# Optimization experiments

Hardware: AMD Instinct MI355X
Metric: run time of the kernel (lower is better)

Reference implementation:

```python
import jax, jax.numpy as jnp
import numpy as np

D_MODEL = 512
N_HEADS = 8
D_FF = 1024
LV = 2048
LT = 512
GAMMA = 0.9
SCALE_BASE = 512  # XPOS default scale_base


def _dup_interleave(m):
    # (L, d/2) -> (L, d) duplicating each column: [a,b] -> [a,a,b,b]
    return jnp.repeat(m, 2, axis=-1)


def _xpos(x, downscale=False):
    # XPOS rotary embedding (RetNet-style), x: (B, L, d)
    B, L, d = x.shape
    half = d // 2
    s = (jnp.arange(0, d, 2, dtype=jnp.float32) + 0.4 * d) / (1.4 * d)  # (d/2,)
    scale = s[None, :] ** (jnp.arange(L, dtype=jnp.float32)[:, None] / SCALE_BASE)  # (L, d/2)
    inv_freq = 1.0 / (10000.0 ** (jnp.arange(half, dtype=jnp.float32) / half))
    ang = jnp.arange(L, dtype=jnp.float32)[:, None] * inv_freq[None, :]  # (L, d/2)
    if downscale:
        scale = 1.0 / scale
    sin = _dup_interleave(jnp.sin(ang) * scale)[None]  # (1, L, d)
    cos = _dup_interleave(jnp.cos(ang) * scale)[None]
    x1, x2 = x[..., 0::2], x[..., 1::2]
    rot = jnp.stack((-x2, x1), axis=-1).reshape(x.shape)  # rotate_every_two
    return x * cos + rot * sin


def _sine_pos(L, d):
    # DETR-style normalized 1D sine position embedding, mask = ones(1, L)
    x_embed = jnp.arange(1, L + 1, dtype=jnp.float32)  # cumsum of ones
    x_embed = x_embed / (x_embed[-1] + 1e-6) * (2.0 * np.pi)
    dim_t = jnp.arange(d, dtype=jnp.float32)
    dim_t = 10000.0 ** (2.0 * jnp.floor(dim_t / 2.0) / d)
    pos = x_embed[:, None] / dim_t[None, :]  # (L, d)
    pos = jnp.stack((jnp.sin(pos[:, 0::2]), jnp.cos(pos[:, 1::2])), axis=2).reshape(L, d)
    return pos[None]  # (1, L, d)


def _ln(x, w, b, eps=1e-5):
    mu = jnp.mean(x, axis=-1, keepdims=True)
    var = jnp.var(x, axis=-1, keepdims=True)
    return (x - mu) / jnp.sqrt(var + eps) * w + b


def _ret_forward(src_vid, src_txt, ln1_w, ln1_b, wq, bq, wk, bk, wv, bv, wo, bo,
                 lin1_w, lin1_b, lin2_w, lin2_b, ln2_w, ln2_b, ln3_w, ln3_b,
                 learn_ret_w):
    B, Lv, D = src_vid.shape
    Lt = src_txt.shape[1]
    h, dk = N_HEADS, D // N_HEADS

    # retention decay matrix D[n,m] = gamma^(n-m) for n>=m else 0
    n = jnp.arange(Lv)
    delta = jnp.maximum(n[:, None] - n[None, :], 0).astype(jnp.float32)
    Dm = jnp.where(n[:, None] >= n[None, :], GAMMA ** delta, 0.0)

    # learned sparse mask
    learn = jax.nn.sigmoid(learn_ret_w.reshape(Lv, Lv))
    diag = jnp.eye(Lv, dtype=jnp.float32)
    video_ret = (1.0 - diag) * learn
    learn_mask = diag + video_ret
    mask = Dm * learn_mask  # mask_choice == 'both'
    loss_sparsity = jnp.mean(jnp.abs(video_ret))

    # position encodings
    pos_vid_q = _xpos(src_vid)
    pos_vid_k = _xpos(src_vid, downscale=True)
    pos_txt = _sine_pos(Lt, D)
    src = jnp.concatenate([src_vid, src_txt], axis=1)       # (B, Lv+Lt, D)
    pos = jnp.concatenate([pos_vid_q, pos_txt], axis=1)
    pos_k = jnp.concatenate([pos_vid_k, pos_txt], axis=1)

    # --- RetLayer (eval mode: dropout = identity) ---
    src2 = _ln(src, ln1_w, ln1_b)
    q = src2[:, :Lv] + pos[:, :Lv]
    k = src2[:, :Lv] + pos_k[:, :Lv]
    v = src2[:, :Lv]

    # multi-head attention with MULTIPLICATIVE mask on logits
    qh = (q @ wq.T + bq).reshape(B, Lv, h, dk) / jnp.sqrt(jnp.float32(dk))
    kh = (k @ wk.T + bk).reshape(B, Lv, h, dk)
    vh = (v @ wv.T + bv).reshape(B, Lv, h, dk)
    attn = jnp.einsum('blhd,bmhd->bhlm', qh, kh) * mask[None, None]
    attn = jax.nn.softmax(attn, axis=-1)
    vid_att = jnp.einsum('bhlm,bmhd->blhd', attn, vh).reshape(B, Lv, D)
    vid_att = vid_att @ wo.T + bo

    src2 = jnp.concatenate([vid_att, src2[:, Lv:]], axis=1) + pos
    src = src + src2
    src2 = _ln(src, ln2_w, ln2_b)
    src2 = jax.nn.gelu(src2 @ lin1_w.T + lin1_b, approximate=False) @ lin2_w.T + lin2_b
    src = src + src2
    src = _ln(src, ln3_w, ln3_b)
    return src[:, :Lv], src[:, Lv:], loss_sparsity


def setup_inputs() -> dict:
    key = jax.random.key(0)
    ks = jax.random.split(key, 12)
    D, F = D_MODEL, D_FF
    w = lambda k, shp: (jax.random.normal(k, shp, dtype=jnp.float32) * 0.02)
    return {
        'src_vid': jax.random.normal(ks[0], (1, LV, D), dtype=jnp.float32),
        'src_txt': jax.random.normal(ks[1], (1, LT, D), dtype=jnp.float32),
        'ln1_w': jnp.ones((D,), jnp.float32), 'ln1_b': jnp.zeros((D,), jnp.float32),
        'wq': w(ks[2], (D, D)), 'bq': jnp.zeros((D,), jnp.float32),
        'wk': w(ks[3], (D, D)), 'bk': jnp.zeros((D,), jnp.float32),
        'wv': w(ks[4], (D, D)), 'bv': jnp.zeros((D,), jnp.float32),
        'wo': w(ks[5], (D, D)), 'bo': jnp.zeros((D,), jnp.float32),
        'lin1_w': w(ks[6], (F, D)), 'lin1_b': jnp.zeros((F,), jnp.float32),
        'lin2_w': w(ks[7], (D, F)), 'lin2_b': jnp.zeros((D,), jnp.float32),
        'ln2_w': jnp.ones((D,), jnp.float32), 'ln2_b': jnp.zeros((D,), jnp.float32),
        'ln3_w': jnp.ones((D,), jnp.float32), 'ln3_b': jnp.zeros((D,), jnp.float32),
        'learn_ret_w': jax.random.normal(ks[8], (LV * LV,), dtype=jnp.float32),
    }


def reference(src_vid, src_txt, ln1_w, ln1_b, wq, bq, wk, bk, wv, bv, wo, bo,
              lin1_w, lin1_b, lin2_w, lin2_b, ln2_w, ln2_b, ln3_w, ln3_b,
              learn_ret_w):
    return _ret_forward(src_vid, src_txt, ln1_w, ln1_b, wq, bq, wk, bk, wv, bv,
                        wo, bo, lin1_w, lin1_b, lin2_w, lin2_b, ln2_w, ln2_b,
                        ln3_w, ln3_b, learn_ret_w)
```

## Files before the change

### kernel.cpp

```cpp
#include <hip/hip_runtime.h>
#include <hip/hip_bf16.h>
#include <math.h>

#define LVID 2048
#define LTXT 512
#define DMOD 512
#define LTOT 2560
#define LOG2_GAMMA (-0.15200309344504995f)
#define LOG2E 1.4426950408889634f

typedef __bf16 bf16x8 __attribute__((ext_vector_type(8)));
typedef float f32x4 __attribute__((ext_vector_type(4)));

__device__ inline f32x4 mfma_bf16(bf16x8 a, bf16x8 b, f32x4 c) {
  return __builtin_amdgcn_mfma_f32_16x16x32_bf16(a, b, c, 0, 0, 0);
}

__device__ inline void gload_lds16(const void* g, void* l) {
  __builtin_amdgcn_global_load_lds(
      (const __attribute__((address_space(1))) void*)g,
      (__attribute__((address_space(3))) void*)l, 16, 0, 0);
}

union U8 { __hip_bfloat16 b[8]; uint4 u; };

__global__ __launch_bounds__(256) void k_prep_ln1(
    const float* __restrict__ lw, float* __restrict__ premask2,
    float* __restrict__ lossp,
    const float* __restrict__ wq, const float* __restrict__ wk,
    const float* __restrict__ wv, const float* __restrict__ wo,
    const float* __restrict__ l1, const float* __restrict__ l2,
    __hip_bfloat16* __restrict__ dst,
    const float* __restrict__ src_vid, const float* __restrict__ src_txt,
    const float* __restrict__ w, const float* __restrict__ b,
    __hip_bfloat16* __restrict__ acat, float* __restrict__ srcA,
    float* __restrict__ posb) {
  int tid = threadIdx.x;
  int blk = blockIdx.x;
  if (blk < 2048) {
    __shared__ float red[256];
    int idx0 = (blk * 256 + tid) * 8;
    int i = idx0 >> 11, j0 = idx0 & 2047;
    float4 lv0 = *(const float4*)&lw[idx0];
    float4 lv1 = *(const float4*)&lw[idx0 + 4];
    float lvv[8] = {lv0.x, lv0.y, lv0.z, lv0.w, lv1.x, lv1.y, lv1.z, lv1.w};
    float pm[8];
    float s = 0.f;
#pragma unroll
    for (int e = 0; e < 8; e++) {
      int j = j0 + e;
      float sig = 1.f / (1.f + __expf(-lvv[e]));
      if (j != i) s += sig;
      float m = (j > i) ? 0.f
              : ((j == i) ? 1.f : exp2f((float)(i - j) * LOG2_GAMMA) * sig);
      pm[e] = m * LOG2E;
    }
    *(float4*)&premask2[idx0]     = *(float4*)&pm[0];
    *(float4*)&premask2[idx0 + 4] = *(float4*)&pm[4];
    red[tid] = s; __syncthreads();
    for (int st = 128; st > 0; st >>= 1) { if (tid < st) red[tid] += red[tid + st]; __syncthreads(); }
    if (tid == 0) lossp[blk] = red[0];
  } else if (blk < 4096) {
    int i4 = (blk - 2048) * 256 + tid;
    const float* sp; int base;
    if (i4 < 131072)      { if (i4 < 65536)  { sp = wq; base = 0; }      else { sp = wk; base = 65536; } }
    else if (i4 < 262144) { if (i4 < 196608) { sp = wv; base = 131072; } else { sp = wo; base = 196608; } }
    else if (i4 < 393216) { sp = l1; base = 262144; }
    else                  { sp = l2; base = 393216; }
    float4 v = ((const float4*)sp)[i4 - base];
    __hip_bfloat16 o[4] = {__float2bfloat16(v.x), __float2bfloat16(v.y),
                           __float2bfloat16(v.z), __float2bfloat16(v.w)};
    *(uint2*)(dst + (size_t)i4 * 4) = *(uint2*)o;
  } else {
    int row = (blk - 4096) * 4 + (tid >> 6);
    int lane = tid & 63;
    const float* xs = (row < LVID) ? (src_vid + (size_t)row * DMOD)
                                   : (src_txt + (size_t)(row - LVID) * DMOD);
    float x[8];
    { float4 v0 = *(const float4*)&xs[lane * 8];
      float4 v1 = *(const float4*)&xs[lane * 8 + 4];
      x[0]=v0.x; x[1]=v0.y; x[2]=v0.z; x[3]=v0.w;
      x[4]=v1.x; x[5]=v1.y; x[6]=v1.z; x[7]=v1.w; }
    float s = 0.f;
#pragma unroll
    for (int i = 0; i < 8; i++) s += x[i];
#pragma unroll
    for (int st = 1; st < 64; st <<= 1) s += __shfl_xor(s, st, 64);
    float mu = s * (1.f / DMOD);
    float vs = 0.f;
#pragma unroll
    for (int i = 0; i < 8; i++) { float d = x[i] - mu; vs += d * d; }
#pragma unroll
    for (int st = 1; st < 64; st <<= 1) vs += __shfl_xor(vs, st, 64);
    float inv = rsqrtf(vs * (1.f / DMOD) + 1e-5f);
    float y[8];
    { float4 w0 = *(const float4*)&w[lane * 8];
      float4 w1 = *(const float4*)&w[lane * 8 + 4];
      float4 b0 = *(const float4*)&b[lane * 8];
      float4 b1 = *(const float4*)&b[lane * 8 + 4];
      float wv_[8] = {w0.x,w0.y,w0.z,w0.w,w1.x,w1.y,w1.z,w1.w};
      float bv_[8] = {b0.x,b0.y,b0.z,b0.w,b1.x,b1.y,b1.z,b1.w};
#pragma unroll
      for (int i = 0; i < 8; i++) y[i] = (x[i] - mu) * inv * wv_[i] + bv_[i]; }
    size_t base = (size_t)row * DMOD + lane * 8;
    if (row < LVID) {
      U8 pv;
#pragma unroll
      for (int i = 0; i < 8; i++) pv.b[i] = __float2bfloat16(y[i]);
      *(uint4*)&acat[(size_t)(4096 + row) * DMOD + lane * 8] = pv.u;
      float pq[8], pk[8];
      float l = (float)row;
#pragma unroll
      for (int p = 0; p < 4; p++) {
        int j = lane * 4 + p;
        float sj = (2.f * j + 204.8f) * (1.f / 716.8f);
        float scale = __powf(sj, l * (1.f / 512.f));
        float invfreq = __powf(10000.f, -(float)j * (1.f / 256.f));
        float sn, cs; __sincosf(l * invfreq, &sn, &cs);
        float cq = cs * scale, sq = sn * scale;
        pq[2*p]   = x[2*p] * cq - x[2*p+1] * sq;
        pq[2*p+1] = x[2*p+1] * cq + x[2*p] * sq;
        float isc = 1.f / scale;
        float ck = cs * isc, sk = sn * isc;
        pk[2*p]   = x[2*p] * ck - x[2*p+1] * sk;
        pk[2*p+1] = x[2*p+1] * ck + x[2*p] * sk;
      }
      *(float4*)&posb[base]     = *(float4*)&pq[0];
      *(float4*)&posb[base + 4] = *(float4*)&pq[4];
      U8 pqv, pkv;
#pragma unroll
      for (int i = 0; i < 8; i++) {
        pqv.b[i] = __float2bfloat16(y[i] + pq[i]);
        pkv.b[i] = __float2bfloat16(y[i] + pk[i]);
      }
      *(uint4*)&acat[(size_t)row * DMOD + lane * 8] = pqv.u;
      *(uint4*)&acat[(size_t)(2048 + row) * DMOD + lane * 8] = pkv.u;
    } else {
      int l = row - LVID;
      float xe = (float)(l + 1) * (6.28318530717958647692f / 512.000001f);
      float o8[8];
#pragma unroll
      for (int p = 0; p < 4; p++) {
        int j = lane * 4 + p;
        float dimt = __powf(10000.f, (float)j * (1.f / 256.f));
        float a = xe / dimt;
        o8[2*p]   = x[2*p]   + y[2*p]   + __sinf(a);
        o8[2*p+1] = x[2*p+1] + y[2*p+1] + __cosf(a);
      }
      *(float4*)&srcA[base]     = *(float4*)&o8[0];
      *(float4*)&srcA[base + 4] = *(float4*)&o8[4];
    }
  }
}

__global__ __launch_bounds__(256) void k_ln2(
    const float* __restrict__ srcA,
    const float* __restrict__ w, const float* __restrict__ b,
    __hip_bfloat16* __restrict__ obf) {
  int row = blockIdx.x * 4 + (threadIdx.x >> 6);
  int lane = threadIdx.x & 63;
  size_t base = (size_t)row * DMOD + lane * 8;
  float x[8];
  { float4 v0 = *(const float4*)&srcA[base];
    float4 v1 = *(const float4*)&srcA[base + 4];
    x[0]=v0.x; x[1]=v0.y; x[2]=v0.z; x[3]=v0.w;
    x[4]=v1.x; x[5]=v1.y; x[6]=v1.z; x[7]=v1.w; }
  float s = 0.f;
#pragma unroll
  for (int i = 0; i < 8; i++) s += x[i];
#pragma unroll
  for (int st = 1; st < 64; st <<= 1) s += __shfl_xor(s, st, 64);
  float mu = s * (1.f / DMOD);
  float vs = 0.f;
#pragma unroll
  for (int i = 0; i < 8; i++) { float d = x[i] - mu; vs += d * d; }
#pragma unroll
  for (int st = 1; st < 64; st <<= 1) vs += __shfl_xor(vs, st, 64);
  float inv = rsqrtf(vs * (1.f / DMOD) + 1e-5f);
  float4 w0 = *(const float4*)&w[lane * 8];
  float4 w1 = *(const float4*)&w[lane * 8 + 4];
  float4 b0 = *(const float4*)&b[lane * 8];
  float4 b1 = *(const float4*)&b[lane * 8 + 4];
  float wv_[8] = {w0.x,w0.y,w0.z,w0.w,w1.x,w1.y,w1.z,w1.w};
  float bv_[8] = {b0.x,b0.y,b0.z,b0.w,b1.x,b1.y,b1.z,b1.w};
  U8 o;
#pragma unroll
  for (int i = 0; i < 8; i++)
    o.b[i] = __float2bfloat16((x[i] - mu) * inv * wv_[i] + bv_[i]);
  *(uint4*)&obf[base] = o.u;
}

__global__ __launch_bounds__(256) void k_ln3(
    const float* __restrict__ srcA, const float* __restrict__ ffo0,
    const float* __restrict__ ffo1,
    const float* __restrict__ w, const float* __restrict__ b,
    float* __restrict__ o, const float* __restrict__ lossp) {
  if (blockIdx.x == 0 && threadIdx.x < 64) {
    float s = 0.f;
    for (int i = threadIdx.x; i < 2048; i += 64) s += lossp[i];
#pragma unroll
    for (int st = 1; st < 64; st <<= 1) s += __shfl_xor(s, st, 64);
    if (threadIdx.x == 0) o[1310720] = s * (1.f / 4194304.f);
  }
  int row = blockIdx.x * 4 + (threadIdx.x >> 6);
  int lane = threadIdx.x & 63;
  size_t base = (size_t)row * DMOD + lane * 8;
  float x[8];
  { float4 a0 = *(const float4*)&srcA[base];
    float4 a1 = *(const float4*)&srcA[base + 4];
    float4 f0 = *(const float4*)&ffo0[base];
    float4 f1 = *(const float4*)&ffo0[base + 4];
    float4 g0 = *(const float4*)&ffo1[base];
    float4 g1 = *(const float4*)&ffo1[base + 4];
    x[0]=a0.x+f0.x+g0.x; x[1]=a0.y+f0.y+g0.y; x[2]=a0.z+f0.z+g0.z; x[3]=a0.w+f0.w+g0.w;
    x[4]=a1.x+f1.x+g1.x; x[5]=a1.y+f1.y+g1.y; x[6]=a1.z+f1.z+g1.z; x[7]=a1.w+f1.w+g1.w; }
  float s = 0.f;
#pragma unroll
  for (int i = 0; i < 8; i++) s += x[i];
#pragma unroll
  for (int st = 1; st < 64; st <<= 1) s += __shfl_xor(s, st, 64);
  float mu = s * (1.f / DMOD);
  float vs = 0.f;
#pragma unroll
  for (int i = 0; i < 8; i++) { float d = x[i] - mu; vs += d * d; }
#pragma unroll
  for (int st = 1; st < 64; st <<= 1) vs += __shfl_xor(vs, st, 64);
  float inv = rsqrtf(vs * (1.f / DMOD) + 1e-5f);
  float4 w0 = *(const float4*)&w[lane * 8];
  float4 w1 = *(const float4*)&w[lane * 8 + 4];
  float4 b0 = *(const float4*)&b[lane * 8];
  float4 b1 = *(const float4*)&b[lane * 8 + 4];
  float wv_[8] = {w0.x,w0.y,w0.z,w0.w,w1.x,w1.y,w1.z,w1.w};
  float bv_[8] = {b0.x,b0.y,b0.z,b0.w,b1.x,b1.y,b1.z,b1.w};
  float y[8];
#pragma unroll
  for (int i = 0; i < 8; i++) y[i] = (x[i] - mu) * inv * wv_[i] + bv_[i];
  *(float4*)&o[base]     = *(float4*)&y[0];
  *(float4*)&o[base + 4] = *(float4*)&y[4];
}

template <int EPI>
__global__ __launch_bounds__(256) void k_gemm4(
    const __hip_bfloat16* __restrict__ A, const __hip_bfloat16* __restrict__ W0,
    const float* __restrict__ b0, const float* __restrict__ b1,
    const float* __restrict__ b2, void* __restrict__ Cv,
    const float* __restrict__ res1, const float* __restrict__ res2,
    float* __restrict__ vtot, int M, int N, int K) {
  __shared__ __hip_bfloat16 sA[2][2048];
  __shared__ __hip_bfloat16 sB[2][2048];
  int tid = threadIdx.x, lane = tid & 63, w = tid >> 6;
  int c16 = lane & 15, q4 = lane >> 4;
  int bm = blockIdx.y * 64, bn = blockIdx.x * 64;
  int seg = (EPI == 3) ? (bm >> 11) : 0;
  const __hip_bfloat16* Wp = (EPI == 3) ? (W0 + (size_t)seg * ((size_t)N * K)) : W0;
  int kb   = (EPI == 5) ? (int)blockIdx.z * (K >> 1) : 0;
  int Keff = (EPI == 5) ? (K >> 1) : K;
  int r0 = tid >> 2, cc0 = (tid & 3) * 8;
  const __hip_bfloat16* gA = A  + (size_t)(bm + r0) * K + kb + cc0;
  const __hip_bfloat16* gB = Wp + (size_t)(bn + r0) * K + kb + cc0;
  auto stage = [&](int buf, int k0) {
    gload_lds16(gA + k0, &sA[buf][(size_t)tid * 8]);
    gload_lds16(gB + k0, &sB[buf][(size_t)tid * 8]);
  };
  f32x4 acc[2][2];
  { f32x4 z = {0.f,0.f,0.f,0.f}; acc[0][0]=z; acc[0][1]=z; acc[1][0]=z; acc[1][1]=z; }
  int wm = w & 1, wn = w >> 1;
  const int S = Keff >> 5;
  stage(0, 0);
  for (int s = 0; s < S; s++) {
    __syncthreads();
    if (s + 1 < S) stage((s + 1) & 1, (s + 1) * 32);
    int bf = s & 1;
    bf16x8 af[2], bfr[2];
    af[0]  = *(const bf16x8*)&sA[bf][(wm*32 + c16) * 32 + q4*8];
    af[1]  = *(const bf16x8*)&sA[bf][(wm*32 + 16 + c16) * 32 + q4*8];
    bfr[0] = *(const bf16x8*)&sB[bf][(wn*32 + c16) * 32 + q4*8];
    bfr[1] = *(const bf16x8*)&sB[bf][(wn*32 + 16 + c16) * 32 + q4*8];
    acc[0][0] = mfma_bf16(af[0], bfr[0], acc[0][0]);
    acc[0][1] = mfma_bf16(af[0], bfr[1], acc[0][1]);
    acc[1][0] = mfma_bf16(af[1], bfr[0], acc[1][0]);
    acc[1][1] = mfma_bf16(af[1], bfr[1], acc[1][1]);
  }
  float alpha = (EPI == 3 && seg == 0) ? 0.125f : 1.f;
  const float* bp = (EPI == 3) ? (seg == 0 ? b0 : (seg == 1 ? b1 : b2)) : b0;
  float vsum[2] = {0.f, 0.f};
#pragma unroll
  for (int j = 0; j < 2; j++) {
    int n = bn + wn*32 + j*16 + c16;
    float bs = bp[n];
    if (EPI == 5 && blockIdx.z != 0) bs = 0.f;
#pragma unroll
    for (int i = 0; i < 2; i++) {
#pragma unroll
      for (int r = 0; r < 4; r++) {
        int m = bm + wm*32 + i*16 + q4*4 + r;
        float v = (acc[i][j][r] + bs) * alpha;
        if (EPI == 4) v = 0.5f * v * (1.f + erff(v * 0.70710678118654752f));
        if (EPI == 2) {
          size_t off = (size_t)m * N + n;
          ((float*)Cv)[off] = v + res1[off] + res2[off];
        } else if (EPI == 4) {
          ((__hip_bfloat16*)Cv)[(size_t)m * N + n] = __float2bfloat16(v);
        } else if (EPI == 5) {
          ((float*)Cv)[(size_t)blockIdx.z * 1310720 + (size_t)m * N + n] = v;
        } else {
          __hip_bfloat16 vb = __float2bfloat16(v);
          ((__hip_bfloat16*)Cv)[(size_t)(m & 2047) * 1536 + seg * 512 + n] = vb;
          if (seg == 2) vsum[j] += __bfloat162float(vb);
        }
      }
    }
  }
  if (EPI == 3 && seg == 2) {
#pragma unroll
    for (int j = 0; j < 2; j++) {
      float s2 = vsum[j];
      s2 += __shfl_xor(s2, 16, 64);
      s2 += __shfl_xor(s2, 32, 64);
      if (q4 == 0) atomicAdd(&vtot[bn + wn*32 + j*16 + c16], s2);
    }
  }
}

__global__ __launch_bounds__(256) void k_attn(
    const __hip_bfloat16* __restrict__ qkv,
    const float* __restrict__ premask2,
    const float* __restrict__ Vtot,
    __hip_bfloat16* __restrict__ outp) {
  __shared__ __hip_bfloat16 sQ[64][72];
  __shared__ __hip_bfloat16 sK[2][64][72];
  __shared__ __hip_bfloat16 sVt[2][64][72];
  __shared__ __hip_bfloat16 sP[64][72];
  __shared__ float sVa[4][64];
  int i0 = blockIdx.x * 64, h = blockIdx.y;
  int tid = threadIdx.x, lane = tid & 63, w = tid >> 6;
  int c16 = lane & 15, q4 = lane >> 4;
  {
    int r = tid >> 2, c0 = (tid & 3) * 16;
    const __hip_bfloat16* g = qkv + (size_t)(i0 + r) * 1536 + h * 64 + c0;
    *(uint4*)&sQ[r][c0]     = *(const uint4*)g;
    *(uint4*)&sQ[r][c0 + 8] = *(const uint4*)(g + 8);
  }
  int thi = i0 >> 6;
  int tlo = (i0 > 900) ? ((i0 - 900) >> 6) : 0;
  float rm = 0.f, rz = 0.f;
  f32x4 O[4];
  { f32x4 z = {0.f,0.f,0.f,0.f}; O[0]=z; O[1]=z; O[2]=z; O[3]=z; }
  float vacc = 0.f;
  int kr = tid >> 2, kc = (tid & 3) * 16;
  uint4 pk0, pk1;
  U8 pv0, pv1;
  {
    const __hip_bfloat16* gk = qkv + (size_t)(tlo*64 + kr) * 1536 + 512 + h*64 + kc;
    pk0 = *(const uint4*)gk; pk1 = *(const uint4*)(gk + 8);
    const __hip_bfloat16* gv = qkv + (size_t)(tlo*64 + w*16) * 1536 + 1024 + h*64 + lane;
#pragma unroll
    for (int j = 0; j < 8; j++) pv0.b[j] = gv[(size_t)j * 1536];
#pragma unroll
    for (int j = 0; j < 8; j++) pv1.b[j] = gv[(size_t)(j + 8) * 1536];
  }
  for (int t = tlo; t <= thi; t++) {
    int buf = (t - tlo) & 1;
    *(uint4*)&sK[buf][kr][kc]       = pk0;
    *(uint4*)&sK[buf][kr][kc + 8]   = pk1;
    *(uint4*)&sVt[buf][lane][w*16]     = pv0.u;
    *(uint4*)&sVt[buf][lane][w*16 + 8] = pv1.u;
#pragma unroll
    for (int j = 0; j < 8; j++) vacc += __bfloat162float(pv0.b[j]);
#pragma unroll
    for (int j = 0; j < 8; j++) vacc += __bfloat162float(pv1.b[j]);
    __syncthreads();
    if (t < thi) {
      const __hip_bfloat16* gk = qkv + (size_t)((t+1)*64 + kr) * 1536 + 512 + h*64 + kc;
      pk0 = *(const uint4*)gk; pk1 = *(const uint4*)(gk + 8);
      const __hip_bfloat16* gv = qkv + (size_t)((t+1)*64 + w*16) * 1536 + 1024 + h*64 + lane;
#pragma unroll
      for (int j = 0; j < 8; j++) pv0.b[j] = gv[(size_t)j * 1536];
#pragma unroll
      for (int j = 0; j < 8; j++) pv1.b[j] = gv[(size_t)(j + 8) * 1536];
    }
    bf16x8 bq0 = *(const bf16x8*)&sQ[w*16 + c16][q4*8];
    bf16x8 bq1 = *(const bf16x8*)&sQ[w*16 + c16][32 + q4*8];
    f32x4 St[4];
#pragma unroll
    for (int jt = 0; jt < 4; jt++) {
      f32x4 z = {0.f,0.f,0.f,0.f};
      bf16x8 a0 = *(const bf16x8*)&sK[buf][jt*16 + c16][q4*8];
      bf16x8 a1 = *(const bf16x8*)&sK[buf][jt*16 + c16][32 + q4*8];
      z = mfma_bf16(a0, bq0, z);
      z = mfma_bf16(a1, bq1, z);
      St[jt] = z;
    }
    int qg = i0 + w*16 + c16;
    float lg[4][4];
    float tmax = -3.0e38f;
#pragma unroll
    for (int jt = 0; jt < 4; jt++) {
      float4 pm = *(const float4*)&premask2[(size_t)qg * 2048 + t*64 + jt*16 + q4*4];
      lg[jt][0] = St[jt][0] * pm.x; lg[jt][1] = St[jt][1] * pm.y;
      lg[jt][2] = St[jt][2] * pm.z; lg[jt][3] = St[jt][3] * pm.w;
#pragma unroll
      for (int r = 0; r < 4; r++) tmax = fmaxf(tmax, lg[jt][r]);
    }
    tmax = fmaxf(tmax, __shfl_xor(tmax, 16, 64));
    tmax = fmaxf(tmax, __shfl_xor(tmax, 32, 64));
    float mn = fmaxf(rm, tmax);
    float al = exp2f(rm - mn);
    rm = mn;
    float zp = 0.f;
#pragma unroll
    for (int jt = 0; jt < 4; jt++) {
      U8 e4;
      float e0 = exp2f(lg[jt][0] - rm), e1 = exp2f(lg[jt][1] - rm);
      float e2 = exp2f(lg[jt][2] - rm), e3 = exp2f(lg[jt][3] - rm);
      zp += e0 + e1 + e2 + e3;
      e4.b[0] = __float2bfloat16(e0); e4.b[1] = __float2bfloat16(e1);
      e4.b[2] = __float2bfloat16(e2); e4.b[3] = __float2bfloat16(e3);
      *(uint2*)&sP[w*16 + c16][jt*16 + q4*4] = *(uint2*)&e4.b[0];
    }
    zp += __shfl_xor(zp, 16, 64);
    zp += __shfl_xor(zp, 32, 64);
    rz = rz * al + zp;
    float alr[4];
#pragma unroll
    for (int r = 0; r < 4; r++) alr[r] = __shfl(al, q4*4 + r, 64);
#pragma unroll
    for (int dt = 0; dt < 4; dt++)
#pragma unroll
      for (int r = 0; r < 4; r++) O[dt][r] *= alr[r];
    bf16x8 ap0 = *(const bf16x8*)&sP[w*16 + c16][q4*8];
    bf16x8 ap1 = *(const bf16x8*)&sP[w*16 + c16][32 + q4*8];
#pragma unroll
    for (int dt = 0; dt < 4; dt++) {
      bf16x8 bv0 = *(const bf16x8*)&sVt[buf][dt*16 + c16][q4*8];
      bf16x8 bv1 = *(const bf16x8*)&sVt[buf][dt*16 + c16][32 + q4*8];
      O[dt] = mfma_bf16(ap0, bv0, O[dt]);
      O[dt] = mfma_bf16(ap1, bv1, O[dt]);
    }
  }
  sVa[w][lane] = vacc;
  __syncthreads();
  float rmr[4], rzr[4];
#pragma unroll
  for (int r = 0; r < 4; r++) {
    rmr[r] = __shfl(rm, q4*4 + r, 64);
    rzr[r] = __shfl(rz, q4*4 + r, 64);
  }
  float nu = (float)(2048 - 64 * (thi - tlo + 1));
#pragma unroll
  for (int dt = 0; dt < 4; dt++) {
    int d = dt*16 + c16;
    float va = sVa[0][d] + sVa[1][d] + sVa[2][d] + sVa[3][d];
    float vu = Vtot[h*64 + d] - va;
#pragma unroll
    for (int r = 0; r < 4; r++) {
      float eu = exp2f(-rmr[r]);
      float o = (O[dt][r] + eu * vu) / (rzr[r] + nu * eu);
      outp[(size_t)(i0 + w*16 + q4*4 + r) * DMOD + h*64 + d] = __float2bfloat16(o);
    }
  }
}

extern "C" void kernel_launch(void* const* d_in, const int* in_sizes, int n_in,
                              void* d_out, int out_size, void* d_ws, size_t ws_size,
                              hipStream_t stream) {
  const float* src_vid = (const float*)d_in[0];
  const float* src_txt = (const float*)d_in[1];
  const float* ln1_w = (const float*)d_in[2];
  const float* ln1_b = (const float*)d_in[3];
  const float* wq = (const float*)d_in[4];
  const float* bq = (const float*)d_in[5];
  const float* wk = (const float*)d_in[6];
  const float* bk = (const float*)d_in[7];
  const float* wv = (const float*)d_in[8];
  const float* bv = (const float*)d_in[9];
  const float* wo = (const float*)d_in[10];
  const float* bo = (const float*)d_in[11];
  const float* lin1_w = (const float*)d_in[12];
  const float* lin1_b = (const float*)d_in[13];
  const float* lin2_w = (const float*)d_in[14];
  const float* lin2_b = (const float*)d_in[15];
  const float* ln2_w = (const float*)d_in[16];
  const float* ln2_b = (const float*)d_in[17];
  const float* ln3_w = (const float*)d_in[18];
  const float* ln3_b = (const float*)d_in[19];
  const float* lw = (const float*)d_in[20];
  float* out = (float*)d_out;

  char* wsb = (char*)d_ws;
  float* premask2       = (float*)(wsb + 0);
  __hip_bfloat16* wqb   = (__hip_bfloat16*)(wsb + 16777216);
  __hip_bfloat16* wob   = wqb + 786432;
  __hip_bfloat16* l1b   = wqb + 1048576;
  __hip_bfloat16* l2b   = wqb + 1572864;
  __hip_bfloat16* acat  = (__hip_bfloat16*)(wsb + 20971520);
  __hip_bfloat16* qkvb  = (__hip_bfloat16*)(wsb + 27262976);
  __hip_bfloat16* vattb = (__hip_bfloat16*)(wsb + 33554432);
  float* srcA           = (float*)(wsb + 35651584);
  float* posb           = (float*)(wsb + 46137344);
  __hip_bfloat16* s2b   = (__hip_bfloat16*)(wsb + 51380224);
  __hip_bfloat16* hidb  = (__hip_bfloat16*)(wsb + 54525952);
  float* ffo0           = (float*)(wsb + 59768832);
  float* ffo1           = (float*)(wsb + 65011712);
  float* Vtot           = (float*)(wsb + 70254592);
  float* lossp          = Vtot + 512;

  hipMemsetAsync(Vtot, 0, 512 * sizeof(float), stream);

  k_prep_ln1<<<4736, 256, 0, stream>>>(lw, premask2, lossp,
      wq, wk, wv, wo, lin1_w, lin2_w, wqb,
      src_vid, src_txt, ln1_w, ln1_b, acat, srcA, posb);

  k_gemm4<3><<<dim3(8, 96), 256, 0, stream>>>(acat, wqb, bq, bk, bv,
      qkvb, nullptr, nullptr, Vtot, 6144, 512, 512);
  k_attn<<<dim3(32, 8), 256, 0, stream>>>(qkvb, premask2, Vtot, vattb);
  k_gemm4<2><<<dim3(8, 32), 256, 0, stream>>>(vattb, wob, bo, nullptr, nullptr,
      srcA, src_vid, posb, nullptr, 2048, 512, 512);
  k_ln2<<<640, 256, 0, stream>>>(srcA, ln2_w, ln2_b, s2b);
  k_gemm4<4><<<dim3(16, 40), 256, 0, stream>>>(s2b, l1b, lin1_b, nullptr, nullptr,
      hidb, nullptr, nullptr, nullptr, 2560, 1024, 512);
  k_gemm4<5><<<dim3(8, 40, 2), 256, 0, stream>>>(hidb, l2b, lin2_b, nullptr, nullptr,
      ffo0, nullptr, nullptr, nullptr, 2560, 512, 1024);
  k_ln3<<<640, 256, 0, stream>>>(srcA, ffo0, ffo1, ln3_w, ln3_b, out, lossp);
}
```

Baseline: 221.2 us.

## Split attention over key tiles with combine kernel, store V transposed, skip unused premask writes

The attention kernel is split into two halves along the key-tile range (grid z=2). Each half writes unnormalized partial outputs plus running max and sum, and a new combine kernel merges them with the uniform-weight contribution from the untouched key tiles. The QKV GEMM epilogue now writes V transposed and accumulates per-tile column sums, replacing the strided per-element V gathers and in-kernel V sums. The prep kernel only writes premask entries inside the band the attention reads. This adds a launch and an intermediate buffer round trip in exchange for doubling attention parallelism and coalesced V loads.

```diff
diff --git a/kernel.cpp b/kernel.cpp
--- a/kernel.cpp
+++ b/kernel.cpp
@@ -39,8 +39,11 @@
   int blk = blockIdx.x;
   if (blk < 2048) {
     __shared__ float red[256];
+    int i = blk;
+    int i0r = i & ~63;
+    int tloCol = (i0r > 900) ? (((i0r - 900) >> 6) << 6) : 0;
     int idx0 = (blk * 256 + tid) * 8;
-    int i = idx0 >> 11, j0 = idx0 & 2047;
+    int j0 = idx0 & 2047;
     float4 lv0 = *(const float4*)&lw[idx0];
     float4 lv1 = *(const float4*)&lw[idx0 + 4];
     float lvv[8] = {lv0.x, lv0.y, lv0.z, lv0.w, lv1.x, lv1.y, lv1.z, lv1.w};
@@ -55,8 +58,10 @@
               : ((j == i) ? 1.f : exp2f((float)(i - j) * LOG2_GAMMA) * sig);
       pm[e] = m * LOG2E;
     }
-    *(float4*)&premask2[idx0]     = *(float4*)&pm[0];
-    *(float4*)&premask2[idx0 + 4] = *(float4*)&pm[4];
+    if (j0 >= tloCol && j0 < i0r + 64) {
+      *(float4*)&premask2[idx0]     = *(float4*)&pm[0];
+      *(float4*)&premask2[idx0 + 4] = *(float4*)&pm[4];
+    }
     red[tid] = s; __syncthreads();
     for (int st = 128; st > 0; st >>= 1) { if (tid < st) red[tid] += red[tid + st]; __syncthreads(); }
     if (tid == 0) lossp[blk] = red[0];
@@ -245,7 +250,8 @@
     const float* __restrict__ b0, const float* __restrict__ b1,
     const float* __restrict__ b2, void* __restrict__ Cv,
     const float* __restrict__ res1, const float* __restrict__ res2,
-    float* __restrict__ vtot, int M, int N, int K) {
+    __hip_bfloat16* __restrict__ vT, float* __restrict__ vts,
+    int M, int N, int K) {
   __shared__ __hip_bfloat16 sA[2][2048];
   __shared__ __hip_bfloat16 sB[2][2048];
   int tid = threadIdx.x, lane = tid & 63, w = tid >> 6;
@@ -283,7 +289,39 @@
   }
   float alpha = (EPI == 3 && seg == 0) ? 0.125f : 1.f;
   const float* bp = (EPI == 3) ? (seg == 0 ? b0 : (seg == 1 ? b1 : b2)) : b0;
-  float vsum[2] = {0.f, 0.f};
+  if (EPI == 3 && seg == 2) {
+    int tile = (bm & 2047) >> 6;
+    float vsum[2] = {0.f, 0.f};
+#pragma unroll
+    for (int j = 0; j < 2; j++) {
+      int n = bn + wn*32 + j*16 + c16;
+      float bs = bp[n];
+#pragma unroll
+      for (int i = 0; i < 2; i++) {
+        ushort4 u; float vv[4];
+#pragma unroll
+        for (int r = 0; r < 4; r++) {
+          __hip_bfloat16 vb = __float2bfloat16(acc[i][j][r] + bs);
+          ((__hip_bfloat16*)&u)[r] = vb;
+          vv[r] = __bfloat162float(vb);
+        }
+        int jj = (bm & 2047) + wm*32 + i*16 + q4*4;
+        *(ushort4*)&vT[(size_t)n * 2048 + jj] = u;
+        vsum[j] += vv[0] + vv[1] + vv[2] + vv[3];
+      }
+    }
+#pragma unroll
+    for (int j = 0; j < 2; j++) {
+      float s2 = vsum[j];
+      s2 += __shfl_xor(s2, 16, 64);
+      s2 += __shfl_xor(s2, 32, 64);
+      int n = bn + wn*32 + j*16 + c16;
+      if (q4 == 0) atomicAdd(&vts[(size_t)(n >> 6) * 2048 + tile * 64 + (n & 63)], s2);
+    }
+    return;
+  }
+  float vdummy;
+  (void)vdummy;
 #pragma unroll
   for (int j = 0; j < 2; j++) {
     int n = bn + wn*32 + j*16 + c16;
@@ -304,92 +342,72 @@
         } else if (EPI == 5) {
           ((float*)Cv)[(size_t)blockIdx.z * 1310720 + (size_t)m * N + n] = v;
         } else {
-          __hip_bfloat16 vb = __float2bfloat16(v);
-          ((__hip_bfloat16*)Cv)[(size_t)(m & 2047) * 1536 + seg * 512 + n] = vb;
-          if (seg == 2) vsum[j] += __bfloat162float(vb);
+          ((__hip_bfloat16*)Cv)[(size_t)(m & 2047) * 1024 + seg * 512 + n] = __float2bfloat16(v);
         }
       }
     }
   }
-  if (EPI == 3 && seg == 2) {
-#pragma unroll
-    for (int j = 0; j < 2; j++) {
-      float s2 = vsum[j];
-      s2 += __shfl_xor(s2, 16, 64);
-      s2 += __shfl_xor(s2, 32, 64);
-      if (q4 == 0) atomicAdd(&vtot[bn + wn*32 + j*16 + c16], s2);
-    }
-  }
 }
 
 __global__ __launch_bounds__(256) void k_attn(
-    const __hip_bfloat16* __restrict__ qkv,
+    const __hip_bfloat16* __restrict__ qkb,
     const float* __restrict__ premask2,
-    const float* __restrict__ Vtot,
-    __hip_bfloat16* __restrict__ outp) {
+    const __hip_bfloat16* __restrict__ vT,
+    __hip_bfloat16* __restrict__ Obuf,
+    float* __restrict__ ml) {
   __shared__ __hip_bfloat16 sQ[64][72];
   __shared__ __hip_bfloat16 sK[2][64][72];
   __shared__ __hip_bfloat16 sVt[2][64][72];
   __shared__ __hip_bfloat16 sP[64][72];
-  __shared__ float sVa[4][64];
-  int i0 = blockIdx.x * 64, h = blockIdx.y;
+  int i0 = blockIdx.x * 64, h = blockIdx.y, z = blockIdx.z;
   int tid = threadIdx.x, lane = tid & 63, w = tid >> 6;
   int c16 = lane & 15, q4 = lane >> 4;
   {
     int r = tid >> 2, c0 = (tid & 3) * 16;
-    const __hip_bfloat16* g = qkv + (size_t)(i0 + r) * 1536 + h * 64 + c0;
+    const __hip_bfloat16* g = qkb + (size_t)(i0 + r) * 1024 + h * 64 + c0;
     *(uint4*)&sQ[r][c0]     = *(const uint4*)g;
     *(uint4*)&sQ[r][c0 + 8] = *(const uint4*)(g + 8);
   }
   int thi = i0 >> 6;
   int tlo = (i0 > 900) ? ((i0 - 900) >> 6) : 0;
+  int n = thi - tlo + 1;
+  int t0 = z ? (tlo + (n >> 1)) : tlo;
+  int t1 = z ? thi : (tlo + (n >> 1) - 1);
   float rm = 0.f, rz = 0.f;
   f32x4 O[4];
-  { f32x4 z = {0.f,0.f,0.f,0.f}; O[0]=z; O[1]=z; O[2]=z; O[3]=z; }
-  float vacc = 0.f;
+  { f32x4 zz = {0.f,0.f,0.f,0.f}; O[0]=zz; O[1]=zz; O[2]=zz; O[3]=zz; }
   int kr = tid >> 2, kc = (tid & 3) * 16;
-  uint4 pk0, pk1;
-  U8 pv0, pv1;
-  {
-    const __hip_bfloat16* gk = qkv + (size_t)(tlo*64 + kr) * 1536 + 512 + h*64 + kc;
+  uint4 pk0, pk1, pv0, pv1;
+  if (t0 <= t1) {
+    const __hip_bfloat16* gk = qkb + (size_t)(t0*64 + kr) * 1024 + 512 + h*64 + kc;
     pk0 = *(const uint4*)gk; pk1 = *(const uint4*)(gk + 8);
-    const __hip_bfloat16* gv = qkv + (size_t)(tlo*64 + w*16) * 1536 + 1024 + h*64 + lane;
-#pragma unroll
-    for (int j = 0; j < 8; j++) pv0.b[j] = gv[(size_t)j * 1536];
-#pragma unroll
-    for (int j = 0; j < 8; j++) pv1.b[j] = gv[(size_t)(j + 8) * 1536];
-  }
-  for (int t = tlo; t <= thi; t++) {
-    int buf = (t - tlo) & 1;
-    *(uint4*)&sK[buf][kr][kc]       = pk0;
-    *(uint4*)&sK[buf][kr][kc + 8]   = pk1;
-    *(uint4*)&sVt[buf][lane][w*16]     = pv0.u;
-    *(uint4*)&sVt[buf][lane][w*16 + 8] = pv1.u;
-#pragma unroll
-    for (int j = 0; j < 8; j++) vacc += __bfloat162float(pv0.b[j]);
-#pragma unroll
-    for (int j = 0; j < 8; j++) vacc += __bfloat162float(pv1.b[j]);
+    const __hip_bfloat16* gv = vT + (size_t)(h*64 + kr) * 2048 + t0*64 + kc;
+    pv0 = *(const uint4*)gv; pv1 = *(const uint4*)(gv + 8);
+  }
+  for (int t = t0; t <= t1; t++) {
+    int buf = (t - t0) & 1;
+    *(uint4*)&sK[buf][kr][kc]      = pk0;
+    *(uint4*)&sK[buf][kr][kc + 8]  = pk1;
+    *(uint4*)&sVt[buf][kr][kc]     = pv0;
+    *(uint4*)&sVt[buf][kr][kc + 8] = pv1;
     __syncthreads();
-    if (t < thi) {
-      const __hip_bfloat16* gk = qkv + (size_t)((t+1)*64 + kr) * 1536 + 512 + h*64 + kc;
+    if (t < t1) {
+      const __hip_bfloat16* gk = qkb + (size_t)((t+1)*64 + kr) * 1024 + 512 + h*64 + kc;
       pk0 = *(const uint4*)gk; pk1 = *(const uint4*)(gk + 8);
-      const __hip_bfloat16* gv = qkv + (size_t)((t+1)*64 + w*16) * 1536 + 1024 + h*64 + lane;
-#pragma unroll
-      for (int j = 0; j < 8; j++) pv0.b[j] = gv[(size_t)j * 1536];
-#pragma unroll
-      for (int j = 0; j < 8; j++) pv1.b[j] = gv[(size_t)(j + 8) * 1536];
+      const __hip_bfloat16* gv = vT + (size_t)(h*64 + kr) * 2048 + (t+1)*64 + kc;
+      pv0 = *(const uint4*)gv; pv1 = *(const uint4*)(gv + 8);
     }
     bf16x8 bq0 = *(const bf16x8*)&sQ[w*16 + c16][q4*8];
     bf16x8 bq1 = *(const bf16x8*)&sQ[w*16 + c16][32 + q4*8];
     f32x4 St[4];
 #pragma unroll
     for (int jt = 0; jt < 4; jt++) {
-      f32x4 z = {0.f,0.f,0.f,0.f};
+      f32x4 zz = {0.f,0.f,0.f,0.f};
       bf16x8 a0 = *(const bf16x8*)&sK[buf][jt*16 + c16][q4*8];
       bf16x8 a1 = *(const bf16x8*)&sK[buf][jt*16 + c16][32 + q4*8];
-      z = mfma_bf16(a0, bq0, z);
-      z = mfma_bf16(a1, bq1, z);
-      St[jt] = z;
+      zz = mfma_bf16(a0, bq0, zz);
+      zz = mfma_bf16(a1, bq1, zz);
+      St[jt] = zz;
     }
     int qg = i0 + w*16 + c16;
     float lg[4][4];
@@ -438,27 +456,78 @@
       O[dt] = mfma_bf16(ap1, bv1, O[dt]);
     }
   }
-  sVa[w][lane] = vacc;
-  __syncthreads();
-  float rmr[4], rzr[4];
-#pragma unroll
-  for (int r = 0; r < 4; r++) {
-    rmr[r] = __shfl(rm, q4*4 + r, 64);
-    rzr[r] = __shfl(rz, q4*4 + r, 64);
-  }
-  float nu = (float)(2048 - 64 * (thi - tlo + 1));
+  __hip_bfloat16* ob = Obuf + (size_t)z * (2048 * 512);
 #pragma unroll
   for (int dt = 0; dt < 4; dt++) {
     int d = dt*16 + c16;
-    float va = sVa[0][d] + sVa[1][d] + sVa[2][d] + sVa[3][d];
-    float vu = Vtot[h*64 + d] - va;
-#pragma unroll
-    for (int r = 0; r < 4; r++) {
-      float eu = exp2f(-rmr[r]);
-      float o = (O[dt][r] + eu * vu) / (rzr[r] + nu * eu);
-      outp[(size_t)(i0 + w*16 + q4*4 + r) * DMOD + h*64 + d] = __float2bfloat16(o);
-    }
-  }
+#pragma unroll
+    for (int r = 0; r < 4; r++)
+      ob[(size_t)(i0 + w*16 + q4*4 + r) * DMOD + h*64 + d] = __float2bfloat16(O[dt][r]);
+  }
+  if (q4 == 0) {
+    size_t mi = (((size_t)z * 8 + h) * 2048 + i0 + w*16 + c16) * 2;
+    ml[mi] = rm; ml[mi + 1] = rz;
+  }
+}
+
+__global__ __launch_bounds__(256) void k_comb(
+    const __hip_bfloat16* __restrict__ Obuf, const float* __restrict__ ml,
+    const float* __restrict__ vts,
+    __hip_bfloat16* __restrict__ outp) {
+  __shared__ float sV[32][64];
+  __shared__ float sS[64];
+  __shared__ float sC[64][4];
+  int i0 = blockIdx.x * 64, h = blockIdx.y;
+  int tid = threadIdx.x;
+  int thi = i0 >> 6;
+  int tlo = (i0 > 900) ? ((i0 - 900) >> 6) : 0;
+  int n = thi - tlo + 1;
+  float nu = (float)(2048 - 64 * n);
+  {
+    const float4* src = (const float4*)(vts + (size_t)h * 2048);
+    ((float4*)&sV[0][0])[tid * 2]     = src[tid * 2];
+    ((float4*)&sV[0][0])[tid * 2 + 1] = src[tid * 2 + 1];
+  }
+  __syncthreads();
+  if (tid < 64) {
+    float s = 0.f;
+    for (int t = 0; t < 32; t++) if (t < tlo || t > thi) s += sV[t][tid];
+    sS[tid] = s;
+  } else if (tid < 128) {
+    int r = tid - 64;
+    int row = i0 + r;
+    float m0 = ml[(((size_t)0 * 8 + h) * 2048 + row) * 2];
+    float l0 = ml[(((size_t)0 * 8 + h) * 2048 + row) * 2 + 1];
+    float m1 = ml[(((size_t)1 * 8 + h) * 2048 + row) * 2];
+    float l1 = ml[(((size_t)1 * 8 + h) * 2048 + row) * 2 + 1];
+    float M = fmaxf(m0, m1);
+    float a0 = exp2f(m0 - M), a1 = exp2f(m1 - M), au = exp2f(-M);
+    float dinv = 1.f / (l0 * a0 + l1 * a1 + nu * au);
+    sC[r][0] = a0 * dinv; sC[r][1] = a1 * dinv; sC[r][2] = au * dinv;
+  }
+  __syncthreads();
+  int r = tid >> 2, dc = (tid & 3) * 16;
+  size_t off = (size_t)(i0 + r) * DMOD + h * 64 + dc;
+  U8 o0a, o0b, o1a, o1b, oa, obb;
+  o0a.u = *(const uint4*)&Obuf[off];
+  o0b.u = *(const uint4*)&Obuf[off + 8];
+  o1a.u = *(const uint4*)&Obuf[(size_t)2048 * 512 + off];
+  o1b.u = *(const uint4*)&Obuf[(size_t)2048 * 512 + off + 8];
+  float c0 = sC[r][0], c1 = sC[r][1], cu = sC[r][2];
+#pragma unroll
+  for (int k = 0; k < 8; k++) {
+    float v = __bfloat162float(o0a.b[k]) * c0 + __bfloat162float(o1a.b[k]) * c1
+            + sS[dc + k] * cu;
+    oa.b[k] = __float2bfloat16(v);
+  }
+#pragma unroll
+  for (int k = 0; k < 8; k++) {
+    float v = __bfloat162float(o0b.b[k]) * c0 + __bfloat162float(o1b.b[k]) * c1
+            + sS[dc + 8 + k] * cu;
+    obb.b[k] = __float2bfloat16(v);
+  }
+  *(uint4*)&outp[off]     = oa.u;
+  *(uint4*)&outp[off + 8] = obb.u;
 }
 
 extern "C" void kernel_launch(void* const* d_in, const int* in_sizes, int n_in,
@@ -487,39 +556,44 @@
   const float* lw = (const float*)d_in[20];
   float* out = (float*)d_out;
 
+  const size_t MB = 1048576;
   char* wsb = (char*)d_ws;
   float* premask2       = (float*)(wsb + 0);
-  __hip_bfloat16* wqb   = (__hip_bfloat16*)(wsb + 16777216);
+  __hip_bfloat16* wqb   = (__hip_bfloat16*)(wsb + 16*MB);
   __hip_bfloat16* wob   = wqb + 786432;
   __hip_bfloat16* l1b   = wqb + 1048576;
   __hip_bfloat16* l2b   = wqb + 1572864;
-  __hip_bfloat16* acat  = (__hip_bfloat16*)(wsb + 20971520);
-  __hip_bfloat16* qkvb  = (__hip_bfloat16*)(wsb + 27262976);
-  __hip_bfloat16* vattb = (__hip_bfloat16*)(wsb + 33554432);
-  float* srcA           = (float*)(wsb + 35651584);
-  float* posb           = (float*)(wsb + 46137344);
-  __hip_bfloat16* s2b   = (__hip_bfloat16*)(wsb + 51380224);
-  __hip_bfloat16* hidb  = (__hip_bfloat16*)(wsb + 54525952);
-  float* ffo0           = (float*)(wsb + 59768832);
-  float* ffo1           = (float*)(wsb + 65011712);
-  float* Vtot           = (float*)(wsb + 70254592);
-  float* lossp          = Vtot + 512;
-
-  hipMemsetAsync(Vtot, 0, 512 * sizeof(float), stream);
+  __hip_bfloat16* acat  = (__hip_bfloat16*)(wsb + 20*MB);
+  __hip_bfloat16* qkb   = (__hip_bfloat16*)(wsb + 26*MB);
+  __hip_bfloat16* vTb   = (__hip_bfloat16*)(wsb + 30*MB);
+  __hip_bfloat16* Obuf  = (__hip_bfloat16*)(wsb + 32*MB);
+  float* mlb            = (float*)(wsb + 36*MB);
+  float* vts            = (float*)(wsb + 37*MB);
+  __hip_bfloat16* vattb = (__hip_bfloat16*)(wsb + 38*MB);
+  float* srcA           = (float*)(wsb + 40*MB);
+  float* posb           = (float*)(wsb + 45*MB);
+  __hip_bfloat16* s2b   = (__hip_bfloat16*)(wsb + 50*MB);
+  __hip_bfloat16* hidb  = (__hip_bfloat16*)(wsb + 53*MB);
+  float* ffo0           = (float*)(wsb + 58*MB);
+  float* ffo1           = (float*)(wsb + 63*MB);
+  float* lossp          = (float*)(wsb + 68*MB);
+
+  hipMemsetAsync(vts, 0, 8 * 32 * 64 * sizeof(float), stream);
 
   k_prep_ln1<<<4736, 256, 0, stream>>>(lw, premask2, lossp,
       wq, wk, wv, wo, lin1_w, lin2_w, wqb,
       src_vid, src_txt, ln1_w, ln1_b, acat, srcA, posb);
 
   k_gemm4<3><<<dim3(8, 96), 256, 0, stream>>>(acat, wqb, bq, bk, bv,
-      qkvb, nullptr, nullptr, Vtot, 6144, 512, 512);
-  k_attn<<<dim3(32, 8), 256, 0, stream>>>(qkvb, premask2, Vtot, vattb);
+      qkb, nullptr, nullptr, vTb, vts, 6144, 512, 512);
+  k_attn<<<dim3(32, 8, 2), 256, 0, stream>>>(qkb, premask2, vTb, Obuf, mlb);
+  k_comb<<<dim3(32, 8), 256, 0, stream>>>(Obuf, mlb, vts, vattb);
   k_gemm4<2><<<dim3(8, 32), 256, 0, stream>>>(vattb, wob, bo, nullptr, nullptr,
-      srcA, src_vid, posb, nullptr, 2048, 512, 512);
+      srcA, src_vid, posb, nullptr, nullptr, 2048, 512, 512);
   k_ln2<<<640, 256, 0, stream>>>(srcA, ln2_w, ln2_b, s2b);
   k_gemm4<4><<<dim3(16, 40), 256, 0, stream>>>(s2b, l1b, lin1_b, nullptr, nullptr,
-      hidb, nullptr, nullptr, nullptr, 2560, 1024, 512);
+      hidb, nullptr, nullptr, nullptr, nullptr, 2560, 1024, 512);
   k_gemm4<5><<<dim3(8, 40, 2), 256, 0, stream>>>(hidb, l2b, lin2_b, nullptr, nullptr,
-      ffo0, nullptr, nullptr, nullptr, 2560, 512, 1024);
+      ffo0, nullptr, nullptr, nullptr, nullptr, 2560, 512, 1024);
   k_ln3<<<640, 256, 0, stream>>>(srcA, ffo0, ffo1, ln3_w, ln3_b, out, lossp);
 }
```

Result: faster. 216.1 us (-2.3%).
